# Kernel tuning notes

Hardware: AMD Instinct MI355X
Metric: run time of the kernel (lower is better)

## Reference

```python
import jax, jax.numpy as jnp
import numpy as np

B, S, E = 20, 4096, 256
BLOCK = 128
LEFT, RIGHT = 1, 1


def setup_inputs() -> dict:
    key = jax.random.key(0)
    ks = jax.random.split(key, 6)
    x = jax.random.normal(ks[0], (B, S, E), dtype=jnp.float32)
    scale = 0.02
    Wq = jax.random.normal(ks[1], (E, E), dtype=jnp.float32) * scale
    Wk = jax.random.normal(ks[2], (E, E), dtype=jnp.float32) * scale
    Wv = jax.random.normal(ks[3], (E, E), dtype=jnp.float32) * scale
    Wo = jax.random.normal(ks[4], (E, E), dtype=jnp.float32) * scale
    bo = jnp.zeros((E,), dtype=jnp.float32)
    return {"x": x, "Wq": Wq, "Wk": Wk, "Wv": Wv, "Wo": Wo, "bo": bo}


def _block_context(blocks, left, right):
    # blocks: [B, nb, bs, E] -> [B, nb, (left+right+1)*bs, E]
    b, nb, bs, e = blocks.shape
    w = left + right + 1
    padded = jnp.pad(blocks, ((0, 0), (left, right), (0, 0), (0, 0)))
    idx = jnp.arange(nb)[:, None] + jnp.arange(w)[None, :]  # [nb, w]
    ctx = padded[:, idx]  # [B, nb, w, bs, E]
    return ctx.reshape(b, nb, w * bs, e)


def reference(x, Wq, Wk, Wv, Wo, bo):
    b, s, e = x.shape
    nb = s // BLOCK
    q = x @ Wq
    k = x @ Wk
    v = x @ Wv
    qb = q.reshape(b, nb, BLOCK, e)
    kb = k.reshape(b, nb, BLOCK, e)
    vb = v.reshape(b, nb, BLOCK, e)
    kc = _block_context(kb, LEFT, RIGHT)  # [B, nb, ctx, E]
    vc = _block_context(vb, LEFT, RIGHT)
    logits = jnp.einsum('bnqd,bnkd->bnqk', qb, kc) / jnp.sqrt(jnp.float32(e))
    attn = jax.nn.softmax(logits, axis=-1)
    out = jnp.einsum('bnqk,bnkd->bnqd', attn, vc)  # [B, nb, bs, E]
    # Faithful to TF: TensorArray.stack() -> [nb, B, bs, E], then reshape to [B, S, E]
    out = jnp.transpose(out, (1, 0, 2, 3)).reshape(b, s, e)
    return out @ Wo + bo
```

## Files before the change

### kernel.cpp

```cpp
#include <hip/hip_runtime.h>
#include <stdint.h>

#define B_   20
#define S_   4096
#define E_   256
#define NB_  32
#define M_   (B_ * S_)

#define OFF_Q   41943040ull
#define OFF_K   83886080ull
#define OFF_V   125829120ull
#define OFF_WT  167772160ull

typedef __attribute__((ext_vector_type(4))) float f32x4;
typedef __attribute__((ext_vector_type(8))) short short8;
typedef __attribute__((ext_vector_type(4))) float float4v;
typedef __attribute__((ext_vector_type(4))) unsigned short us4;

__device__ __forceinline__ unsigned short f2bf(float f) {
  unsigned int u = __builtin_bit_cast(unsigned int, f);
  u += 0x7FFFu + ((u >> 16) & 1u);
  return (unsigned short)(u >> 16);
}

__device__ __forceinline__ void glds16(const void* g, void* l) {
  __builtin_amdgcn_global_load_lds(
      (const __attribute__((address_space(1))) unsigned int*)g,
      (__attribute__((address_space(3))) unsigned int*)l, 16, 0, 0);
}

__global__ void k_convert_x(const float* __restrict__ x, unsigned short* __restrict__ xb) {
  size_t id = (size_t)blockIdx.x * 256 + threadIdx.x;
  float4v v = *(const float4v*)(x + id * 4);
  us4 o;
  o[0] = f2bf(v[0]); o[1] = f2bf(v[1]); o[2] = f2bf(v[2]); o[3] = f2bf(v[3]);
  *(us4*)(xb + id * 4) = o;
}

__global__ void k_convert_w(const float* __restrict__ Wq, const float* __restrict__ Wk,
                            const float* __restrict__ Wv, const float* __restrict__ Wo,
                            unsigned short* __restrict__ WT) {
  __shared__ float T[64][65];
  int g = blockIdx.x;
  int m = g >> 4, t = g & 15;
  int k0 = (t >> 2) * 64, n0 = (t & 3) * 64;
  const float* src = (m == 0) ? Wq : (m == 1) ? Wk : (m == 2) ? Wv : Wo;
  unsigned short* dst = WT + (size_t)m * 65536;
  int tid = threadIdx.x;
#pragma unroll
  for (int it = 0; it < 4; ++it) {
    int idx = it * 256 + tid;
    int kr = idx >> 4, nc = idx & 15;
    float4v v = *(const float4v*)(src + (size_t)(k0 + kr) * 256 + n0 + nc * 4);
    T[kr][nc * 4 + 0] = v[0]; T[kr][nc * 4 + 1] = v[1];
    T[kr][nc * 4 + 2] = v[2]; T[kr][nc * 4 + 3] = v[3];
  }
  __syncthreads();
#pragma unroll
  for (int it = 0; it < 2; ++it) {
    int idx = it * 256 + tid;
    int nr = idx >> 3, kc = idx & 7;
    short8 o;
#pragma unroll
    for (int e = 0; e < 8; ++e) o[e] = (short)f2bf(T[kc * 8 + e][nr]);
    *(short8*)(dst + (size_t)(n0 + nr) * 256 + k0 + kc * 8) = o;
  }
}

__global__ __launch_bounds__(256, 2) void k_gemm(const unsigned short* __restrict__ A,
                                                 const unsigned short* __restrict__ WT,
                                                 unsigned short* __restrict__ qk,
                                                 unsigned short* __restrict__ vT) {
  __shared__ char Alds[2][16384];
  __shared__ char Blds[2][16384];
  int g = blockIdx.x;
  int xcd = g & 7, idx = g >> 3;
  int rt = xcd * 80 + idx / 6;
  int ct = idx % 6;
  int mat = ct >> 1;
  int col0 = (ct & 1) * 128;

  int tid = threadIdx.x, w = tid >> 6, l = tid & 63;
  int wr = (w >> 1) * 64, wc = (w & 1) * 64;
  int hi16 = (l >> 4) * 16;

  const char* Ab = (const char*)A + (size_t)rt * 128 * 512;
  const char* Bb = (const char*)(WT + (size_t)mat * 65536) + (size_t)col0 * 512;

  auto STAGE = [&](int bufi, int s) {
    int k0b = s * 128;
#pragma unroll
    for (int j8 = 0; j8 < 4; ++j8) {
      int d = (j8 * 256 + tid) * 16;
      int row = d >> 7;
      int cx = (d & 127) ^ ((row & 7) << 4);
      glds16(Ab + (size_t)row * 512 + k0b + cx, Alds[bufi] + d);
      glds16(Bb + (size_t)row * 512 + k0b + cx, Blds[bufi] + d);
    }
  };

  f32x4 acc[4][4] = {};
  STAGE(0, 0);

  for (int s = 0; s < 4; ++s) {
    int cur = s & 1;
    if (s < 3) {
      STAGE(cur ^ 1, s + 1);
      asm volatile("s_waitcnt vmcnt(8)" ::: "memory");
    } else {
      asm volatile("s_waitcnt vmcnt(0)" ::: "memory");
    }
    __builtin_amdgcn_sched_barrier(0);
    __builtin_amdgcn_s_barrier();
#pragma unroll
    for (int ks = 0; ks < 2; ++ks) {
      short8 a[4], bb[4];
#pragma unroll
      for (int i = 0; i < 4; ++i) {
        int ra = wr + 16 * i + (l & 15);
        a[i] = *(const short8*)(Alds[cur] + ra * 128 + ((ks * 64 + hi16) ^ ((ra & 7) << 4)));
        int rb = wc + 16 * i + (l & 15);
        bb[i] = *(const short8*)(Blds[cur] + rb * 128 + ((rb & 7) << 4 ^ (ks * 64 + hi16)));
      }
      __builtin_amdgcn_s_setprio(1);
#pragma unroll
      for (int i = 0; i < 4; ++i)
#pragma unroll
        for (int j = 0; j < 4; ++j)
          acc[i][j] = __builtin_amdgcn_mfma_f32_16x16x32_bf16(a[i], bb[j], acc[i][j], 0, 0, 0);
      __builtin_amdgcn_s_setprio(0);
    }
    asm volatile("s_waitcnt lgkmcnt(0)" ::: "memory");
    __builtin_amdgcn_sched_barrier(0);
    __builtin_amdgcn_s_barrier();
  }

  if (mat < 2) {
    unsigned short* oq = qk + (size_t)mat * M_ * 256;
#pragma unroll
    for (int i = 0; i < 4; ++i)
#pragma unroll
      for (int j = 0; j < 4; ++j)
#pragma unroll
        for (int r = 0; r < 4; ++r) {
          int row = rt * 128 + wr + 16 * i + (l >> 4) * 4 + r;
          int col = col0 + wc + 16 * j + (l & 15);
          oq[(size_t)row * 256 + col] = f2bf(acc[i][j][r]);
        }
  } else {
#pragma unroll
    for (int i = 0; i < 4; ++i) {
      int row0 = rt * 128 + wr + 16 * i + (l >> 4) * 4;
      int b = row0 >> 12, s0 = row0 & 4095;
#pragma unroll
      for (int j = 0; j < 4; ++j) {
        int col = col0 + wc + 16 * j + (l & 15);
        us4 o;
#pragma unroll
        for (int r = 0; r < 4; ++r) o[r] = f2bf(acc[i][j][r]);
        *(us4*)(vT + ((size_t)(b * 256 + col) << 12) + s0) = o;
      }
    }
  }
}

__global__ __launch_bounds__(256, 2) void k_attn(const unsigned short* __restrict__ q,
                                                 const unsigned short* __restrict__ k,
                                                 const unsigned short* __restrict__ vT,
                                                 const unsigned short* __restrict__ WT,
                                                 const float* __restrict__ bo,
                                                 float* __restrict__ out) {
  __shared__ char kb2[2][32768];
  __shared__ char pl[64 * 144];

  int g = blockIdx.x;
  int xcd = g & 7, idx = g >> 3;
  int nbid = xcd * 80 + (idx >> 1);
  int half = idx & 1;
  int b = nbid >> 5, n = nbid & 31;
  int tid = threadIdx.x, w = tid >> 6, l = tid & 63;
  int hi16 = (l >> 4) * 16;

  int rowbase = b * 4096 + n * 128 + half * 64 + w * 16;
  const char* qrow = (const char*)q + (size_t)(rowbase + (l & 15)) * 512;
  short8 qf[8];
#pragma unroll
  for (int ks = 0; ks < 8; ++ks) qf[ks] = *(const short8*)(qrow + ks * 64 + hi16);

  f32x4 zero4 = {0.f, 0.f, 0.f, 0.f};
  f32x4 oacc[16];
#pragma unroll
  for (int fj = 0; fj < 16; ++fj) oacc[fj] = zero4;
  float einit = (n == 0 || n == 31) ? 8.0f : 0.0f;
  float dsum[4] = {einit, einit, einit, einit};

  const char* kbase = (const char*)k + (size_t)b * 4096 * 512;
  const char* vtb   = (const char*)vT + (size_t)b * 256 * 8192;
  const char* woT   = (const char*)(WT + 3 * 65536);

  int c0 = (n == 0) ? 2 : 0;
  int c1 = (n == 31) ? 3 : 5;
  int P = (c1 - c0 + 1) * 2;

  auto STAGE = [&](int bufi, int p) {
    int c = c0 + (p >> 1);
    int kg = (n + (c >> 1) - 1) * 128 + (c & 1) * 64;
    char* dst = kb2[bufi];
    if ((p & 1) == 0) {
#pragma unroll
      for (int j8 = 0; j8 < 8; ++j8) {
        int d = (j8 * 256 + tid) * 16;
        int key = d >> 9;
        int f2 = (d & 511) ^ ((key & 7) << 4);
        glds16(kbase + (size_t)(kg + key) * 512 + f2, dst + d);
      }
    } else {
#pragma unroll
      for (int j8 = 0; j8 < 8; ++j8) {
        int d = (j8 * 256 + tid) * 16;
        int feat = d >> 7;
        int kx = (d & 127) ^ ((feat & 7) << 4);
        glds16(vtb + (size_t)feat * 8192 + (size_t)kg * 2 + kx, dst + d);
      }
    }
  };

  STAGE(0, 0);

  for (int p = 0; p < P; ++p) {
    int cur = p & 1;
    if (p + 1 < P) {
      STAGE(cur ^ 1, p + 1);
      asm volatile("s_waitcnt vmcnt(8)" ::: "memory");
    } else {
      asm volatile("s_waitcnt vmcnt(0)" ::: "memory");
    }
    __builtin_amdgcn_sched_barrier(0);
    __builtin_amdgcn_s_barrier();

    const char* kv = kb2[cur];
    if ((p & 1) == 0) {
#pragma unroll
      for (int j = 0; j < 4; ++j) {
        f32x4 s = zero4;
        int key = 16 * j + (l & 15);
        int kb0 = key * 512, km = (key & 7) << 4;
        __builtin_amdgcn_s_setprio(1);
#pragma unroll
        for (int ks = 0; ks < 8; ++ks) {
          short8 kf = *(const short8*)(kv + kb0 + ((ks * 64 + hi16) ^ km));
          s = __builtin_amdgcn_mfma_f32_16x16x32_bf16(qf[ks], kf, s, 0, 0, 0);
        }
        __builtin_amdgcn_s_setprio(0);
#pragma unroll
        for (int r = 0; r < 4; ++r) {
          float pv = __expf(s[r] * 0.0625f);
          dsum[r] += pv;
          int prow = w * 16 + (l >> 4) * 4 + r;
          *(unsigned short*)(pl + prow * 144 + key * 2) = f2bf(pv);
        }
      }
    } else {
#pragma unroll
      for (int ks2 = 0; ks2 < 2; ++ks2) {
        short8 pa = *(const short8*)(pl + (w * 16 + (l & 15)) * 144 + ks2 * 64 + hi16);
        __builtin_amdgcn_s_setprio(1);
#pragma unroll
        for (int fj = 0; fj < 16; ++fj) {
          int feat = 16 * fj + (l & 15);
          short8 vf = *(const short8*)(kv + feat * 128 + ((ks2 * 64 + hi16) ^ ((feat & 7) << 4)));
          oacc[fj] = __builtin_amdgcn_mfma_f32_16x16x32_bf16(pa, vf, oacc[fj], 0, 0, 0);
        }
        __builtin_amdgcn_s_setprio(0);
      }
    }
    asm volatile("s_waitcnt lgkmcnt(0)" ::: "memory");
    __builtin_amdgcn_sched_barrier(0);
    __builtin_amdgcn_s_barrier();
  }

#pragma unroll
  for (int r = 0; r < 4; ++r) {
    float t = dsum[r];
    t += __shfl_xor(t, 1); t += __shfl_xor(t, 2);
    t += __shfl_xor(t, 4); t += __shfl_xor(t, 8);
    dsum[r] = 1.0f / t;
  }

  char* OL = kb2[0];
#pragma unroll
  for (int fj = 0; fj < 16; ++fj) {
    int c2 = 2 * (16 * fj + (l & 15));
#pragma unroll
    for (int r = 0; r < 4; ++r) {
      int qr = w * 16 + (l >> 4) * 4 + r;
      *(unsigned short*)(OL + qr * 512 + (c2 ^ ((qr & 7) << 4))) =
          f2bf(oacc[fj][r] * dsum[r]);
    }
  }

  auto STAGE_WO = [&](int kc) {
#pragma unroll
    for (int j8 = 0; j8 < 8; ++j8) {
      int d = (j8 * 256 + tid) * 16;
      int nrow = d >> 7;
      int kx = (d & 127) ^ ((nrow & 7) << 4);
      glds16(woT + (size_t)nrow * 512 + kc * 128 + kx, kb2[1] + d);
    }
  };

  f32x4 acc2[16];
#pragma unroll
  for (int j = 0; j < 16; ++j) acc2[j] = zero4;

  STAGE_WO(0);
  for (int kc = 0; kc < 4; ++kc) {
    asm volatile("s_waitcnt vmcnt(0)" ::: "memory");
    __builtin_amdgcn_sched_barrier(0);
    __builtin_amdgcn_s_barrier();
#pragma unroll
    for (int kstep = 0; kstep < 2; ++kstep) {
      int qr = w * 16 + (l & 15);
      short8 af = *(const short8*)(OL + qr * 512 +
                    ((kc * 128 + kstep * 64 + hi16) ^ ((qr & 7) << 4)));
      __builtin_amdgcn_s_setprio(1);
#pragma unroll
      for (int j = 0; j < 16; ++j) {
        int nr = 16 * j + (l & 15);
        short8 bf = *(const short8*)(kb2[1] + nr * 128 +
                      ((kstep * 64 + hi16) ^ ((nr & 7) << 4)));
        acc2[j] = __builtin_amdgcn_mfma_f32_16x16x32_bf16(af, bf, acc2[j], 0, 0, 0);
      }
      __builtin_amdgcn_s_setprio(0);
    }
    asm volatile("s_waitcnt lgkmcnt(0)" ::: "memory");
    __builtin_amdgcn_sched_barrier(0);
    __builtin_amdgcn_s_barrier();
    if (kc < 3) STAGE_WO(kc + 1);
  }

  int f0 = n * 2560 + b * 128 + half * 64 + w * 16 + (l >> 4) * 4;
#pragma unroll
  for (int j = 0; j < 16; ++j) {
    int col = 16 * j + (l & 15);
    float bj = bo[col];
#pragma unroll
    for (int r = 0; r < 4; ++r)
      out[(size_t)(f0 + r) * 256 + col] = acc2[j][r] + bj;
  }
}

extern "C" void kernel_launch(void* const* d_in, const int* in_sizes, int n_in,
                              void* d_out, int out_size, void* d_ws, size_t ws_size,
                              hipStream_t stream) {
  (void)in_sizes; (void)n_in; (void)out_size; (void)ws_size;
  const float* x  = (const float*)d_in[0];
  const float* Wq = (const float*)d_in[1];
  const float* Wk = (const float*)d_in[2];
  const float* Wv = (const float*)d_in[3];
  const float* Wo = (const float*)d_in[4];
  const float* bo = (const float*)d_in[5];

  char* ws = (char*)d_ws;
  unsigned short* xb = (unsigned short*)ws;
  unsigned short* qb = (unsigned short*)(ws + OFF_Q);
  unsigned short* kb = (unsigned short*)(ws + OFF_K);
  unsigned short* vT = (unsigned short*)(ws + OFF_V);
  unsigned short* WT = (unsigned short*)(ws + OFF_WT);

  k_convert_x<<<20480, 256, 0, stream>>>(x, xb);
  k_convert_w<<<64, 256, 0, stream>>>(Wq, Wk, Wv, Wo, WT);
  k_gemm<<<3840, 256, 0, stream>>>(xb, WT, qb, vT);
  k_attn<<<1280, 256, 0, stream>>>(qb, kb, vT, WT, bo, (float*)d_out);
}
```

Before: 293.3 us.

## Fuse x bf16 conversion into QKV GEMM with register-resident A tiles

Removes the separate fp32-to-bf16 conversion kernel for x. Each QKV block now loads its 128-row x tile straight from fp32 global memory into bf16 registers once, then loops over all six output column tiles while streaming only the weight tiles through LDS. Outputs are staged through a swizzled LDS buffer so global stores are coalesced 16-byte writes for both q/k and transposed v. The goal is to avoid writing and re-reading the bf16 copy of x and to cut redundant A reloads, at the cost of fewer blocks (640), more register pressure, and serial column tiles per block.

New measurement: 307.5 us. +4.8%, slower.

```diff
diff --git a/kernel.cpp b/kernel.cpp
--- a/kernel.cpp
+++ b/kernel.cpp
@@ -27,14 +27,6 @@
   __builtin_amdgcn_global_load_lds(
       (const __attribute__((address_space(1))) unsigned int*)g,
       (__attribute__((address_space(3))) unsigned int*)l, 16, 0, 0);
-}
-
-__global__ void k_convert_x(const float* __restrict__ x, unsigned short* __restrict__ xb) {
-  size_t id = (size_t)blockIdx.x * 256 + threadIdx.x;
-  float4v v = *(const float4v*)(x + id * 4);
-  us4 o;
-  o[0] = f2bf(v[0]); o[1] = f2bf(v[1]); o[2] = f2bf(v[2]); o[3] = f2bf(v[3]);
-  *(us4*)(xb + id * 4) = o;
 }
 
 __global__ void k_convert_w(const float* __restrict__ Wq, const float* __restrict__ Wk,
@@ -67,98 +59,140 @@
   }
 }
 
-__global__ __launch_bounds__(256, 2) void k_gemm(const unsigned short* __restrict__ A,
-                                                 const unsigned short* __restrict__ WT,
-                                                 unsigned short* __restrict__ qk,
-                                                 unsigned short* __restrict__ vT) {
-  __shared__ char Alds[2][16384];
-  __shared__ char Blds[2][16384];
+__global__ __launch_bounds__(256, 2) void k_qkv(const float* __restrict__ x,
+                                                const unsigned short* __restrict__ WT,
+                                                unsigned short* __restrict__ qk,
+                                                unsigned short* __restrict__ vT) {
+  __shared__ char Bl[2][16384];
+  __shared__ char Cl[32768];
+
   int g = blockIdx.x;
-  int xcd = g & 7, idx = g >> 3;
-  int rt = xcd * 80 + idx / 6;
-  int ct = idx % 6;
-  int mat = ct >> 1;
-  int col0 = (ct & 1) * 128;
-
+  int rt = (g & 7) * 80 + (g >> 3);
   int tid = threadIdx.x, w = tid >> 6, l = tid & 63;
-  int wr = (w >> 1) * 64, wc = (w & 1) * 64;
+  int wr = w * 32;
   int hi16 = (l >> 4) * 16;
-
-  const char* Ab = (const char*)A + (size_t)rt * 128 * 512;
-  const char* Bb = (const char*)(WT + (size_t)mat * 65536) + (size_t)col0 * 512;
-
-  auto STAGE = [&](int bufi, int s) {
-    int k0b = s * 128;
-#pragma unroll
-    for (int j8 = 0; j8 < 4; ++j8) {
-      int d = (j8 * 256 + tid) * 16;
+  const char* WTc = (const char*)WT;
+
+  short8 a[2][8];
+  const float* xb0 = x + (size_t)rt * 128 * 256;
+#pragma unroll
+  for (int i = 0; i < 2; ++i) {
+    const float* xr = xb0 + (size_t)(wr + 16 * i + (l & 15)) * 256 + (l >> 4) * 8;
+#pragma unroll
+    for (int ks = 0; ks < 8; ++ks) {
+      float4v v0 = *(const float4v*)(xr + ks * 32);
+      float4v v1 = *(const float4v*)(xr + ks * 32 + 4);
+      short8 t;
+      t[0] = (short)f2bf(v0[0]); t[1] = (short)f2bf(v0[1]);
+      t[2] = (short)f2bf(v0[2]); t[3] = (short)f2bf(v0[3]);
+      t[4] = (short)f2bf(v1[0]); t[5] = (short)f2bf(v1[1]);
+      t[6] = (short)f2bf(v1[2]); t[7] = (short)f2bf(v1[3]);
+      a[i][ks] = t;
+    }
+  }
+
+  auto STAGE_B = [&](int ct, int s, int bufi) {
+    const char* Bb = WTc + (ct >> 1) * 131072 + (ct & 1) * 65536;
+    char* dst = Bl[bufi];
+#pragma unroll
+    for (int j4 = 0; j4 < 4; ++j4) {
+      int d = (j4 * 256 + tid) * 16;
       int row = d >> 7;
       int cx = (d & 127) ^ ((row & 7) << 4);
-      glds16(Ab + (size_t)row * 512 + k0b + cx, Alds[bufi] + d);
-      glds16(Bb + (size_t)row * 512 + k0b + cx, Blds[bufi] + d);
+      glds16(Bb + (size_t)row * 512 + s * 128 + cx, dst + d);
     }
   };
 
-  f32x4 acc[4][4] = {};
-  STAGE(0, 0);
-
-  for (int s = 0; s < 4; ++s) {
-    int cur = s & 1;
-    if (s < 3) {
-      STAGE(cur ^ 1, s + 1);
-      asm volatile("s_waitcnt vmcnt(8)" ::: "memory");
+  STAGE_B(0, 0, 0);
+
+#pragma unroll
+  for (int ct = 0; ct < 6; ++ct) {
+    f32x4 acc[2][8];
+#pragma unroll
+    for (int i = 0; i < 2; ++i)
+#pragma unroll
+      for (int j = 0; j < 8; ++j) acc[i][j] = (f32x4){0.f, 0.f, 0.f, 0.f};
+
+#pragma unroll
+    for (int s = 0; s < 4; ++s) {
+      int u = ct * 4 + s;
+      if (u < 23) {
+        STAGE_B((u + 1) >> 2, (u + 1) & 3, (u + 1) & 1);
+        asm volatile("s_waitcnt vmcnt(4)" ::: "memory");
+      } else {
+        asm volatile("s_waitcnt vmcnt(0)" ::: "memory");
+      }
+      __builtin_amdgcn_sched_barrier(0);
+      __builtin_amdgcn_s_barrier();
+      const char* bl = Bl[u & 1];
+#pragma unroll
+      for (int ksl = 0; ksl < 2; ++ksl) {
+        short8 bfr[8];
+#pragma unroll
+        for (int j = 0; j < 8; ++j) {
+          int rb = 16 * j + (l & 15);
+          bfr[j] = *(const short8*)(bl + rb * 128 + ((ksl * 64 + hi16) ^ ((rb & 7) << 4)));
+        }
+        __builtin_amdgcn_s_setprio(1);
+#pragma unroll
+        for (int i = 0; i < 2; ++i)
+#pragma unroll
+          for (int j = 0; j < 8; ++j)
+            acc[i][j] = __builtin_amdgcn_mfma_f32_16x16x32_bf16(a[i][s * 2 + ksl], bfr[j],
+                                                                acc[i][j], 0, 0, 0);
+        __builtin_amdgcn_s_setprio(0);
+      }
+      asm volatile("s_waitcnt lgkmcnt(0)" ::: "memory");
+      __builtin_amdgcn_sched_barrier(0);
+      __builtin_amdgcn_s_barrier();
+    }
+
+    int mat = ct >> 1, col0 = (ct & 1) * 128;
+    if (mat < 2) {
+#pragma unroll
+      for (int i = 0; i < 2; ++i)
+#pragma unroll
+        for (int j = 0; j < 8; ++j) {
+          int colL = 16 * j + (l & 15);
+#pragma unroll
+          for (int r = 0; r < 4; ++r) {
+            int rowL = wr + 16 * i + (l >> 4) * 4 + r;
+            *(unsigned short*)(Cl + rowL * 256 + ((2 * colL) ^ ((rowL & 7) << 4))) =
+                f2bf(acc[i][j][r]);
+          }
+        }
     } else {
-      asm volatile("s_waitcnt vmcnt(0)" ::: "memory");
-    }
-    __builtin_amdgcn_sched_barrier(0);
-    __builtin_amdgcn_s_barrier();
-#pragma unroll
-    for (int ks = 0; ks < 2; ++ks) {
-      short8 a[4], bb[4];
-#pragma unroll
-      for (int i = 0; i < 4; ++i) {
-        int ra = wr + 16 * i + (l & 15);
-        a[i] = *(const short8*)(Alds[cur] + ra * 128 + ((ks * 64 + hi16) ^ ((ra & 7) << 4)));
-        int rb = wc + 16 * i + (l & 15);
-        bb[i] = *(const short8*)(Blds[cur] + rb * 128 + ((rb & 7) << 4 ^ (ks * 64 + hi16)));
-      }
-      __builtin_amdgcn_s_setprio(1);
-#pragma unroll
-      for (int i = 0; i < 4; ++i)
-#pragma unroll
-        for (int j = 0; j < 4; ++j)
-          acc[i][j] = __builtin_amdgcn_mfma_f32_16x16x32_bf16(a[i], bb[j], acc[i][j], 0, 0, 0);
-      __builtin_amdgcn_s_setprio(0);
+#pragma unroll
+      for (int i = 0; i < 2; ++i)
+#pragma unroll
+        for (int j = 0; j < 8; ++j) {
+          int rowL0 = wr + 16 * i + (l >> 4) * 4;
+          int colL = 16 * j + (l & 15);
+          us4 o;
+#pragma unroll
+          for (int r = 0; r < 4; ++r) o[r] = f2bf(acc[i][j][r]);
+          *(us4*)(Cl + colL * 256 + ((2 * rowL0) ^ ((colL & 7) << 4))) = o;
+        }
     }
     asm volatile("s_waitcnt lgkmcnt(0)" ::: "memory");
     __builtin_amdgcn_sched_barrier(0);
     __builtin_amdgcn_s_barrier();
-  }
-
-  if (mat < 2) {
-    unsigned short* oq = qk + (size_t)mat * M_ * 256;
-#pragma unroll
-    for (int i = 0; i < 4; ++i)
-#pragma unroll
-      for (int j = 0; j < 4; ++j)
-#pragma unroll
-        for (int r = 0; r < 4; ++r) {
-          int row = rt * 128 + wr + 16 * i + (l >> 4) * 4 + r;
-          int col = col0 + wc + 16 * j + (l & 15);
-          oq[(size_t)row * 256 + col] = f2bf(acc[i][j][r]);
-        }
-  } else {
-#pragma unroll
-    for (int i = 0; i < 4; ++i) {
-      int row0 = rt * 128 + wr + 16 * i + (l >> 4) * 4;
-      int b = row0 >> 12, s0 = row0 & 4095;
-#pragma unroll
-      for (int j = 0; j < 4; ++j) {
-        int col = col0 + wc + 16 * j + (l & 15);
-        us4 o;
-#pragma unroll
-        for (int r = 0; r < 4; ++r) o[r] = f2bf(acc[i][j][r]);
-        *(us4*)(vT + ((size_t)(b * 256 + col) << 12) + s0) = o;
+    {
+      int o = tid >> 1, h = tid & 1;
+      const char* crow = Cl + o * 256;
+      char* gdst;
+      if (mat < 2) {
+        gdst = (char*)qk + (size_t)mat * M_ * 512 + (size_t)(rt * 128 + o) * 512 +
+               col0 * 2 + h * 128;
+      } else {
+        int b = rt >> 5;
+        gdst = (char*)vT + (size_t)(b * 256 + col0 + o) * 8192 +
+               (size_t)(rt & 31) * 256 + h * 128;
+      }
+#pragma unroll
+      for (int i16 = 0; i16 < 8; ++i16) {
+        short8 v = *(const short8*)(crow + ((h * 128 + i16 * 16) ^ ((o & 7) << 4)));
+        *(short8*)(gdst + i16 * 16) = v;
       }
     }
   }
@@ -362,14 +396,12 @@
   const float* bo = (const float*)d_in[5];
 
   char* ws = (char*)d_ws;
-  unsigned short* xb = (unsigned short*)ws;
   unsigned short* qb = (unsigned short*)(ws + OFF_Q);
   unsigned short* kb = (unsigned short*)(ws + OFF_K);
   unsigned short* vT = (unsigned short*)(ws + OFF_V);
   unsigned short* WT = (unsigned short*)(ws + OFF_WT);
 
-  k_convert_x<<<20480, 256, 0, stream>>>(x, xb);
   k_convert_w<<<64, 256, 0, stream>>>(Wq, Wk, Wv, Wo, WT);
-  k_gemm<<<3840, 256, 0, stream>>>(xb, WT, qb, vT);
+  k_qkv<<<640, 256, 0, stream>>>(x, WT, qb, vT);
   k_attn<<<1280, 256, 0, stream>>>(qb, kb, vT, WT, bo, (float*)d_out);
 }
```

## Shrink attention LDS footprint, read V and Wo directly from global for higher occupancy

Applied to the files above, without the earlier changes.

The attention kernel now stages only K in LDS, in smaller 32-key chunks with half-size double buffers. V^T and the output projection weights Wo are read straight from global memory into MFMA operands instead of being staged in LDS. The launch bound is raised from 2 to 4 blocks per CU. The aim is to cut LDS usage and barrier traffic so more waves fit per CU. The cost is more loop iterations and uncoalesced per-lane global loads of V and Wo, and register pressure at the higher occupancy target may cause spills. LDS now holds 32 KB of K buffers plus 5 KB for P, down from 64 KB plus 9 KB. The 64x256 bf16 output tile is written into both K buffers back to back, which the 512-byte row stride fits.

After: 526.7 us. 1.8x slower.

```diff
diff --git a/kernel.cpp b/kernel.cpp
--- a/kernel.cpp
+++ b/kernel.cpp
@@ -164,14 +164,14 @@
   }
 }
 
-__global__ __launch_bounds__(256, 2) void k_attn(const unsigned short* __restrict__ q,
+__global__ __launch_bounds__(256, 4) void k_attn(const unsigned short* __restrict__ q,
                                                  const unsigned short* __restrict__ k,
                                                  const unsigned short* __restrict__ vT,
                                                  const unsigned short* __restrict__ WT,
                                                  const float* __restrict__ bo,
                                                  float* __restrict__ out) {
-  __shared__ char kb2[2][32768];
-  __shared__ char pl[64 * 144];
+  __shared__ char kb2[2][16384];
+  __shared__ char pl[64 * 80];
 
   int g = blockIdx.x;
   int xcd = g & 7, idx = g >> 3;
@@ -198,40 +198,28 @@
   const char* vtb   = (const char*)vT + (size_t)b * 256 * 8192;
   const char* woT   = (const char*)(WT + 3 * 65536);
 
-  int c0 = (n == 0) ? 2 : 0;
-  int c1 = (n == 31) ? 3 : 5;
-  int P = (c1 - c0 + 1) * 2;
-
-  auto STAGE = [&](int bufi, int p) {
-    int c = c0 + (p >> 1);
-    int kg = (n + (c >> 1) - 1) * 128 + (c & 1) * 64;
+  int c0 = (n == 0) ? 4 : 0;
+  int c1 = (n == 31) ? 7 : 11;
+
+  auto STAGE_K = [&](int bufi, int c) {
+    int kg = (n - 1) * 128 + c * 32;
     char* dst = kb2[bufi];
-    if ((p & 1) == 0) {
-#pragma unroll
-      for (int j8 = 0; j8 < 8; ++j8) {
-        int d = (j8 * 256 + tid) * 16;
-        int key = d >> 9;
-        int f2 = (d & 511) ^ ((key & 7) << 4);
-        glds16(kbase + (size_t)(kg + key) * 512 + f2, dst + d);
-      }
-    } else {
-#pragma unroll
-      for (int j8 = 0; j8 < 8; ++j8) {
-        int d = (j8 * 256 + tid) * 16;
-        int feat = d >> 7;
-        int kx = (d & 127) ^ ((feat & 7) << 4);
-        glds16(vtb + (size_t)feat * 8192 + (size_t)kg * 2 + kx, dst + d);
-      }
+#pragma unroll
+    for (int j4 = 0; j4 < 4; ++j4) {
+      int d = (j4 * 256 + tid) * 16;
+      int key = d >> 9;
+      int f2 = (d & 511) ^ ((key & 7) << 4);
+      glds16(kbase + (size_t)(kg + key) * 512 + f2, dst + d);
     }
   };
 
-  STAGE(0, 0);
-
-  for (int p = 0; p < P; ++p) {
-    int cur = p & 1;
-    if (p + 1 < P) {
-      STAGE(cur ^ 1, p + 1);
-      asm volatile("s_waitcnt vmcnt(8)" ::: "memory");
+  STAGE_K(c0 & 1, c0);
+
+  for (int c = c0; c <= c1; ++c) {
+    int cur = c & 1;
+    if (c < c1) {
+      STAGE_K(cur ^ 1, c + 1);
+      asm volatile("s_waitcnt vmcnt(4)" ::: "memory");
     } else {
       asm volatile("s_waitcnt vmcnt(0)" ::: "memory");
     }
@@ -239,40 +227,41 @@
     __builtin_amdgcn_s_barrier();
 
     const char* kv = kb2[cur];
-    if ((p & 1) == 0) {
-#pragma unroll
-      for (int j = 0; j < 4; ++j) {
-        f32x4 s = zero4;
-        int key = 16 * j + (l & 15);
-        int kb0 = key * 512, km = (key & 7) << 4;
-        __builtin_amdgcn_s_setprio(1);
-#pragma unroll
-        for (int ks = 0; ks < 8; ++ks) {
-          short8 kf = *(const short8*)(kv + kb0 + ((ks * 64 + hi16) ^ km));
-          s = __builtin_amdgcn_mfma_f32_16x16x32_bf16(qf[ks], kf, s, 0, 0, 0);
-        }
-        __builtin_amdgcn_s_setprio(0);
-#pragma unroll
-        for (int r = 0; r < 4; ++r) {
-          float pv = __expf(s[r] * 0.0625f);
-          dsum[r] += pv;
-          int prow = w * 16 + (l >> 4) * 4 + r;
-          *(unsigned short*)(pl + prow * 144 + key * 2) = f2bf(pv);
-        }
-      }
-    } else {
-#pragma unroll
-      for (int ks2 = 0; ks2 < 2; ++ks2) {
-        short8 pa = *(const short8*)(pl + (w * 16 + (l & 15)) * 144 + ks2 * 64 + hi16);
-        __builtin_amdgcn_s_setprio(1);
-#pragma unroll
-        for (int fj = 0; fj < 16; ++fj) {
-          int feat = 16 * fj + (l & 15);
-          short8 vf = *(const short8*)(kv + feat * 128 + ((ks2 * 64 + hi16) ^ ((feat & 7) << 4)));
-          oacc[fj] = __builtin_amdgcn_mfma_f32_16x16x32_bf16(pa, vf, oacc[fj], 0, 0, 0);
-        }
-        __builtin_amdgcn_s_setprio(0);
-      }
+#pragma unroll
+    for (int j = 0; j < 2; ++j) {
+      f32x4 s = zero4;
+      int key = 16 * j + (l & 15);
+      int kb0 = key * 512, km = (key & 7) << 4;
+      __builtin_amdgcn_s_setprio(1);
+#pragma unroll
+      for (int ks = 0; ks < 8; ++ks) {
+        short8 kf = *(const short8*)(kv + kb0 + ((ks * 64 + hi16) ^ km));
+        s = __builtin_amdgcn_mfma_f32_16x16x32_bf16(qf[ks], kf, s, 0, 0, 0);
+      }
+      __builtin_amdgcn_s_setprio(0);
+#pragma unroll
+      for (int r = 0; r < 4; ++r) {
+        float pv = __expf(s[r] * 0.0625f);
+        dsum[r] += pv;
+        int prow = w * 16 + (l >> 4) * 4 + r;
+        *(unsigned short*)(pl + prow * 80 + key * 2) = f2bf(pv);
+      }
+    }
+    asm volatile("s_waitcnt lgkmcnt(0)" ::: "memory");
+    __builtin_amdgcn_sched_barrier(0);
+
+    {
+      int kg = (n - 1) * 128 + c * 32;
+      short8 pa = *(const short8*)(pl + (w * 16 + (l & 15)) * 80 + hi16);
+      const char* vcol = vtb + (size_t)(kg + (l >> 4) * 8) * 2;
+      __builtin_amdgcn_s_setprio(1);
+#pragma unroll
+      for (int fj = 0; fj < 16; ++fj) {
+        int feat = 16 * fj + (l & 15);
+        short8 vf = *(const short8*)(vcol + (size_t)feat * 8192);
+        oacc[fj] = __builtin_amdgcn_mfma_f32_16x16x32_bf16(pa, vf, oacc[fj], 0, 0, 0);
+      }
+      __builtin_amdgcn_s_setprio(0);
     }
     asm volatile("s_waitcnt lgkmcnt(0)" ::: "memory");
     __builtin_amdgcn_sched_barrier(0);
@@ -287,7 +276,7 @@
     dsum[r] = 1.0f / t;
   }
 
-  char* OL = kb2[0];
+  char* OL = &kb2[0][0];
 #pragma unroll
   for (int fj = 0; fj < 16; ++fj) {
     int c2 = 2 * (16 * fj + (l & 15));
@@ -298,45 +287,28 @@
           f2bf(oacc[fj][r] * dsum[r]);
     }
   }
-
-  auto STAGE_WO = [&](int kc) {
-#pragma unroll
-    for (int j8 = 0; j8 < 8; ++j8) {
-      int d = (j8 * 256 + tid) * 16;
-      int nrow = d >> 7;
-      int kx = (d & 127) ^ ((nrow & 7) << 4);
-      glds16(woT + (size_t)nrow * 512 + kc * 128 + kx, kb2[1] + d);
-    }
-  };
+  asm volatile("s_waitcnt lgkmcnt(0)" ::: "memory");
+  __builtin_amdgcn_sched_barrier(0);
+
+  short8 af[8];
+  {
+    int qr = w * 16 + (l & 15);
+#pragma unroll
+    for (int ks = 0; ks < 8; ++ks)
+      af[ks] = *(const short8*)(OL + qr * 512 + ((ks * 64 + hi16) ^ ((qr & 7) << 4)));
+  }
 
   f32x4 acc2[16];
 #pragma unroll
   for (int j = 0; j < 16; ++j) acc2[j] = zero4;
-
-  STAGE_WO(0);
-  for (int kc = 0; kc < 4; ++kc) {
-    asm volatile("s_waitcnt vmcnt(0)" ::: "memory");
-    __builtin_amdgcn_sched_barrier(0);
-    __builtin_amdgcn_s_barrier();
-#pragma unroll
-    for (int kstep = 0; kstep < 2; ++kstep) {
-      int qr = w * 16 + (l & 15);
-      short8 af = *(const short8*)(OL + qr * 512 +
-                    ((kc * 128 + kstep * 64 + hi16) ^ ((qr & 7) << 4)));
-      __builtin_amdgcn_s_setprio(1);
-#pragma unroll
-      for (int j = 0; j < 16; ++j) {
-        int nr = 16 * j + (l & 15);
-        short8 bf = *(const short8*)(kb2[1] + nr * 128 +
-                      ((kstep * 64 + hi16) ^ ((nr & 7) << 4)));
-        acc2[j] = __builtin_amdgcn_mfma_f32_16x16x32_bf16(af, bf, acc2[j], 0, 0, 0);
-      }
-      __builtin_amdgcn_s_setprio(0);
-    }
-    asm volatile("s_waitcnt lgkmcnt(0)" ::: "memory");
-    __builtin_amdgcn_sched_barrier(0);
-    __builtin_amdgcn_s_barrier();
-    if (kc < 3) STAGE_WO(kc + 1);
+#pragma unroll
+  for (int kc = 0; kc < 8; ++kc) {
+#pragma unroll
+    for (int j = 0; j < 16; ++j) {
+      int nr = 16 * j + (l & 15);
+      short8 bf = *(const short8*)(woT + (size_t)nr * 512 + kc * 64 + hi16);
+      acc2[j] = __builtin_amdgcn_mfma_f32_16x16x32_bf16(af[kc], bf, acc2[j], 0, 0, 0);
+    }
   }
 
   int f0 = n * 2560 + b * 128 + half * 64 + w * 16 + (l >> 4) * 4;
```
